# Kernel tuning notes

Measured on AMD Instinct MI355X. Metric: run time of the kernel, lower is better.

The kernel has to match this reference:

```python
import jax, jax.numpy as jnp
import numpy as np
from math import sqrt

B, MAXM, DIM, NH, QD, H, W = 8, 4, 128, 8, 16, 16, 16


def _pos_enc(h, w, max_m):
    # SE(2) positional phases: exp(i*m*theta_ij) for relative position j-i on the grid.
    ys, xs = jnp.meshgrid(jnp.arange(h, dtype=jnp.float32), jnp.arange(w, dtype=jnp.float32), indexing='ij')
    coords = jnp.stack([ys.ravel(), xs.ravel()], axis=-1)  # (N, 2)
    d = coords[None, :, :] - coords[:, None, :]            # (N, N, 2) = p_j - p_i
    theta = jnp.arctan2(d[..., 0], d[..., 1])              # (N, N)
    m = jnp.arange(max_m, dtype=jnp.float32)[:, None, None]
    return jnp.exp(1j * m * theta)                         # (max_m, N, N) complex64


def setup_inputs() -> dict:
    key = jax.random.key(0)
    ks = jax.random.split(key, 8)
    mk = lambda k, s: jax.random.normal(k, s, dtype=jnp.float32)
    return {
        'x_re': mk(ks[0], (B, MAXM, DIM, H, W)),
        'x_im': mk(ks[1], (B, MAXM, DIM, H, W)),
        'emb_re': mk(ks[2], (3, 1, MAXM, NH, QD, DIM)),
        'emb_im': mk(ks[3], (3, 1, MAXM, NH, QD, DIM)),
        'enc_re': mk(ks[4], (2, MAXM, NH, 1, QD, 1)),
        'enc_im': mk(ks[5], (2, MAXM, NH, 1, QD, 1)),
        'out_re': mk(ks[6], (MAXM, DIM, NH * QD)),
        'out_im': mk(ks[7], (MAXM, DIM, NH * QD)),
    }


def reference(x_re, x_im, emb_re, emb_im, enc_re, enc_im, out_re, out_im):
    x = (x_re + 1j * x_im)                         # (B, M, D, H, W) complex64
    b, m_, d_, h, w = x.shape
    n = h * w
    x = x.reshape(b, m_, d_, n)                    # (B, M, D, N)
    emb = (emb_re + 1j * emb_im)[:, 0]             # (3, M, NH, QD, D)
    enc = enc_re + 1j * enc_im                     # (2, M, NH, 1, QD, 1)
    w_out = out_re + 1j * out_im                   # (M, D, NH*QD)

    # E = embeddings @ x  -> (3, B, M, NH, QD, N)
    E = jnp.einsum('tmhqD,bmDn->tbmhqn', emb, x)
    E0, K, V = E[0], E[1], E[2]
    Q = jnp.conj(jnp.swapaxes(E0, -2, -1))         # (B, M, NH, N, QD)

    A = jnp.einsum('bmhiq,bmhqj->bmhij', Q, K)     # (B, M, NH, N, N)

    pe = _pos_enc(h, w, m_)                        # (M, N, N)
    enc0 = enc[0, :, :, 0, :, 0]                   # (M, NH, QD)
    enc1 = enc[1, :, :, 0, :, 0]                   # (M, NH, QD)
    # (Q.unsqueeze(-2) @ pos[0]).squeeze(-2) with pos[0][m,h,i,q,j] = enc0[m,h,q]*pe[m,i,j]
    QE = jnp.einsum('bmhiq,mhq->bmhi', Q, enc0)
    A = A + QE[..., None] * pe[None, :, None, :, :]

    A = jnp.sum(A, axis=1)                         # (B, NH, N, N)
    Aw = jax.nn.softmax(jnp.abs(A) / sqrt(QD), axis=-1).astype(jnp.complex64)
    # dropout is identity (eval / p effectively off for the reference)

    res = jnp.einsum('bmhqj,bhij->bmhqi', V, Aw)   # V @ A^T -> (B, M, NH, QD, N)
    # (pos[1] @ A.unsqueeze(-1)).squeeze(-1).T with pos[1][m,h,i,q,j] = enc1[m,h,q]*pe[m,i,j]
    PA = jnp.einsum('mij,bhij->bmhi', pe, Aw)
    res = res + enc1[None, :, :, :, None] * PA[:, :, :, None, :]

    res = res.reshape(b, m_, NH * QD, n)
    out = jnp.einsum('mDk,bmkn->bmDn', w_out, res).reshape(b, m_, d_, h, w)
    return jnp.stack([out.real, out.imag])         # (2, B, M, D, H, W) float32
```

## Files before the change

### kernel.cpp

```cpp
#include <hip/hip_runtime.h>
#include <math.h>

#define BB   8
#define MM   4
#define DD   128
#define NHH  8
#define QDD  16
#define NN   256
#define KO   128

typedef __attribute__((ext_vector_type(8))) short bf16x8;
typedef __attribute__((ext_vector_type(4))) float f32x4;

__device__ inline unsigned short f2bf(float f) {
    union { float f; unsigned u; } v; v.f = f;
    unsigned r = v.u + 0x7FFF + ((v.u >> 16) & 1);
    return (unsigned short)(r >> 16);
}
__device__ inline float bf2f(unsigned short h) {
    union { unsigned u; float f; } v; v.u = ((unsigned)h) << 16;
    return v.f;
}
__device__ inline void bfsplit(float x, unsigned short& hi, unsigned short& lo) {
    hi = f2bf(x);
    lo = f2bf(x - bf2f(hi));
}
__device__ inline bf16x8 derive_im(bf16x8 v) {
    union { bf16x8 v; unsigned u[4]; } in, out;
    in.v = v;
#pragma unroll
    for (int w = 0; w < 4; ++w)
        out.u[w] = ((in.u[w] >> 16) ^ 0x8000u) | (in.u[w] << 16);
    return out.v;
}
__device__ inline bf16x8 derive_im2(bf16x8 v) {
    union { bf16x8 v; unsigned u[4]; } in, out;
    in.v = v;
#pragma unroll
    for (int w = 0; w < 4; ++w)
        out.u[w] = (in.u[w] >> 16) | ((in.u[w] ^ 0x8000u) << 16);
    return out.v;
}

__global__ void pe_kernel(float2* __restrict__ peIJ) {
    int bid = blockIdx.x;
    int m = bid >> 8;
    int i = bid & 255;
    int j = threadIdx.x;
    float dy = (float)((j >> 4) - (i >> 4));
    float dx = (float)((j & 15) - (i & 15));
    float r2 = dx * dx + dy * dy;
    float c1 = 1.f, s1 = 0.f;
    if (r2 > 0.f) {
        float rinv = rsqrtf(r2);
        c1 = dx * rinv; s1 = dy * rinv;
    }
    float c = 1.f, s = 0.f;
    for (int k = 0; k < m; ++k) {
        float nc = c * c1 - s * s1;
        s = c * s1 + s * c1;
        c = nc;
    }
    peIJ[(m * NN + i) * NN + j] = make_float2(c, s);
}

__global__ void convAB_kernel(const float* __restrict__ er, const float* __restrict__ ei,
                              const float* __restrict__ xr, const float* __restrict__ xi,
                              const float* __restrict__ wor, const float* __restrict__ woi,
                              unsigned int* __restrict__ AbfHi, unsigned int* __restrict__ AbfLo,
                              unsigned int* __restrict__ BreHi, unsigned int* __restrict__ BreLo,
                              unsigned int* __restrict__ WFrag) {
    if (blockIdx.x < 96) {
        int tmh = blockIdx.x;
        int base = tmh * QDD * DD;
#pragma unroll
        for (int it = 0; it < 8; ++it) {
            int idx = threadIdx.x + it * 256;
            float ar = er[base + idx];
            float ai = ei[base + idx];
            unsigned short arh, arl, aih, ail;
            bfsplit(ar, arh, arl);
            bfsplit(ai, aih, ail);
            AbfHi[base + idx] = (unsigned int)arh | ((unsigned int)aih << 16);
            AbfLo[base + idx] = (unsigned int)arl | ((unsigned int)ail << 16);
        }
        return;
    }
    if (blockIdx.x >= 352) {
        int c = blockIdx.x - 352;
        int m = c >> 4;
        int dt = (c >> 1) & 7;
        int kshalf = c & 1;
        int tid = threadIdx.x;
        int wav = tid >> 6, lane = tid & 63;
        int ks = kshalf * 4 + wav;
        int D = dt * 16 + (lane & 15);
        unsigned int uu[8];
#pragma unroll
        for (int r = 0; r < 8; ++r) {
            int K2 = ks * 32 + ((lane >> 4) * 8) + r;
            int k = K2 >> 1;
            float v = (K2 & 1) ? woi[(m * DD + D) * KO + k] : wor[(m * DD + D) * KO + k];
            unsigned short hh, ll;
            bfsplit(v, hh, ll);
            uu[r] = (unsigned int)hh | ((unsigned int)ll << 16);
        }
        unsigned int* wp = WFrag + (((size_t)(m * 8 + dt) * 8 + ks) * 64 + lane) * 8;
        *(uint4*)wp = make_uint4(uu[0], uu[1], uu[2], uu[3]);
        *(uint4*)(wp + 4) = make_uint4(uu[4], uu[5], uu[6], uu[7]);
        return;
    }
    int bid = blockIdx.x - 96;
    int bm = bid >> 3;
    int Dg = bid & 7;
    int D0 = Dg * 16;
    int tid = threadIdx.x;

    __shared__ float sxr[16][257];
    __shared__ float sxi[16][257];

    const float* xrp = xr + (size_t)bm * DD * NN;
    const float* xip = xi + (size_t)bm * DD * NN;
#pragma unroll
    for (int it = 0; it < 16; ++it) {
        int i2 = tid + it * 256;
        int r = i2 >> 8, c = i2 & 255;
        sxr[r][c] = xrp[(size_t)(D0 + r) * NN + c];
        sxi[r][c] = xip[(size_t)(D0 + r) * NN + c];
    }
    __syncthreads();

    int n = tid;
    unsigned int reh[16], rel_[16];
#pragma unroll
    for (int d = 0; d < 16; ++d) {
        float br = sxr[d][n];
        float bi = sxi[d][n];
        unsigned short brh, brl, bih, bil;
        bfsplit(br, brh, brl);
        bfsplit(bi, bih, bil);
        reh[d]  = (unsigned int)brh | ((unsigned int)(bih ^ 0x8000) << 16);
        rel_[d] = (unsigned int)brl | ((unsigned int)(bil ^ 0x8000) << 16);
    }
    size_t ob = (size_t)bm * 32768 + (size_t)n * 128 + D0;
#pragma unroll
    for (int w = 0; w < 4; ++w) {
        ((uint4*)(BreHi + ob))[w] = make_uint4(reh[4*w], reh[4*w+1], reh[4*w+2], reh[4*w+3]);
        ((uint4*)(BreLo + ob))[w] = make_uint4(rel_[4*w], rel_[4*w+1], rel_[4*w+2], rel_[4*w+3]);
    }
}

__global__ __launch_bounds__(256, 2)
void e_mfma_kernel(const unsigned short* __restrict__ AbfHi,
                   const unsigned short* __restrict__ AbfLo,
                   const unsigned short* __restrict__ BreHi,
                   const unsigned short* __restrict__ BreLo,
                   const float* __restrict__ encr, const float* __restrict__ enci,
                   float2* __restrict__ E,
                   float2* __restrict__ QE,
                   unsigned int* __restrict__ EaHi, unsigned int* __restrict__ EaLo,
                   unsigned int* __restrict__ KbHi, unsigned int* __restrict__ KbLo) {
    int bid = blockIdx.x;
    int xcd = bid & 7;
    int idx = bid >> 3;
    int pair = xcd * 4 + (idx & 3);
    int h = (idx >> 2) & 7;
    int nhalf = idx >> 5;
    int b = pair >> 2, m = pair & 3;
    int tid = threadIdx.x;
    int wav = tid >> 6, lane = tid & 63;
    int lo = lane & 15, hi = lane >> 4;

    const unsigned short* AH[3];
    const unsigned short* AL[3];
#pragma unroll
    for (int t = 0; t < 3; ++t) {
        size_t aoff = ((size_t)((t * MM + m) * NHH + h)) * QDD * 256;
        AH[t] = AbfHi + aoff;
        AL[t] = AbfLo + aoff;
    }
    size_t boff = (size_t)pair * 256 * 256;
    const unsigned short* BrH = BreHi + boff;
    const unsigned short* BrL = BreLo + boff;

    f32x4 accRe[3][2], accIm[3][2];
#pragma unroll
    for (int t = 0; t < 3; ++t)
#pragma unroll
        for (int nt = 0; nt < 2; ++nt) {
            accRe[t][nt] = (f32x4)(0.f);
            accIm[t][nt] = (f32x4)(0.f);
        }

#pragma unroll
    for (int ks = 0; ks < 8; ++ks) {
        int k0 = ks * 32;
        int arow = lo * 256 + k0 + hi * 8;
        bf16x8 aH[3], aL[3];
#pragma unroll
        for (int t = 0; t < 3; ++t) {
            aH[t] = *(const bf16x8*)(AH[t] + arow);
            aL[t] = *(const bf16x8*)(AL[t] + arow);
        }
#pragma unroll
        for (int nt = 0; nt < 2; ++nt) {
            int n0 = nhalf * 128 + (wav * 2 + nt) * 16;
            size_t brow = (size_t)(n0 + lo) * 256 + k0 + hi * 8;
            bf16x8 brh = *(const bf16x8*)(BrH + brow);
            bf16x8 brl = *(const bf16x8*)(BrL + brow);
            bf16x8 bih = derive_im(brh);
            bf16x8 bil = derive_im(brl);
#pragma unroll
            for (int t = 0; t < 3; ++t) {
                accRe[t][nt] = __builtin_amdgcn_mfma_f32_16x16x32_bf16(aH[t], brh, accRe[t][nt], 0, 0, 0);
                accRe[t][nt] = __builtin_amdgcn_mfma_f32_16x16x32_bf16(aH[t], brl, accRe[t][nt], 0, 0, 0);
                accRe[t][nt] = __builtin_amdgcn_mfma_f32_16x16x32_bf16(aL[t], brh, accRe[t][nt], 0, 0, 0);
                accIm[t][nt] = __builtin_amdgcn_mfma_f32_16x16x32_bf16(aH[t], bih, accIm[t][nt], 0, 0, 0);
                accIm[t][nt] = __builtin_amdgcn_mfma_f32_16x16x32_bf16(aH[t], bil, accIm[t][nt], 0, 0, 0);
                accIm[t][nt] = __builtin_amdgcn_mfma_f32_16x16x32_bf16(aL[t], bih, accIm[t][nt], 0, 0, 0);
            }
        }
    }

    int bh = b * NHH + h;

    {
        float cr[4], ci[4];
#pragma unroll
        for (int reg = 0; reg < 4; ++reg) {
            int q = hi * 4 + reg;
            int eb = (m * NHH + h) * QDD + q;
            cr[reg] = encr[eb];
            ci[reg] = enci[eb];
        }
#pragma unroll
        for (int nt = 0; nt < 2; ++nt) {
            int n0 = nhalf * 128 + (wav * 2 + nt) * 16;
            float sr = 0.f, si = 0.f;
#pragma unroll
            for (int reg = 0; reg < 4; ++reg) {
                float erv = accRe[0][nt][reg];
                float eiv = accIm[0][nt][reg];
                sr = fmaf(erv, cr[reg], fmaf( eiv, ci[reg], sr));
                si = fmaf(erv, ci[reg], fmaf(-eiv, cr[reg], si));
            }
            sr += __shfl_xor(sr, 16); si += __shfl_xor(si, 16);
            sr += __shfl_xor(sr, 32); si += __shfl_xor(si, 32);
            if (hi == 0)
                QE[(size_t)((b * MM + m) * NHH + h) * NN + n0 + lo] = make_float2(sr, si);
        }
    }

#pragma unroll
    for (int t = 0; t < 3; ++t) {
        size_t ebase = (size_t)((((t * BB + b) * MM + m) * NHH + h) * QDD) * NN;
#pragma unroll
        for (int nt = 0; nt < 2; ++nt) {
            int n0 = nhalf * 128 + (wav * 2 + nt) * 16;
            if (t == 2) {
#pragma unroll
                for (int reg = 0; reg < 4; ++reg) {
                    int q = hi * 4 + reg;
                    E[ebase + (size_t)q * NN + n0 + lo] =
                        make_float2(accRe[t][nt][reg], accIm[t][nt][reg]);
                }
            }
            if (t < 2) {
                unsigned int hiU[4], loU[4];
#pragma unroll
                for (int reg = 0; reg < 4; ++reg) {
                    unsigned short rh, rl, ih, il;
                    bfsplit(accRe[t][nt][reg], rh, rl);
                    bfsplit(accIm[t][nt][reg], ih, il);
                    hiU[reg] = (unsigned int)rh | ((unsigned int)ih << 16);
                    loU[reg] = (unsigned int)rl | ((unsigned int)il << 16);
                }
                int r = n0 >> 4;
                size_t fo = (size_t)bh * 16384 + (size_t)((r * 4 + m) * 64 + lane) * 4;
                unsigned int* tH = (t == 0) ? EaHi : KbHi;
                unsigned int* tL = (t == 0) ? EaLo : KbLo;
                *(uint4*)(tH + fo) = make_uint4(hiU[0], hiU[1], hiU[2], hiU[3]);
                *(uint4*)(tL + fo) = make_uint4(loU[0], loU[1], loU[2], loU[3]);
            }
        }
    }
}

__global__ __launch_bounds__(256)
void score_kernel(const unsigned short* __restrict__ EaHi,
                  const unsigned short* __restrict__ EaLo,
                  const unsigned short* __restrict__ KbHi,
                  const unsigned short* __restrict__ KbLo,
                  const float2* __restrict__ QE,
                  const float2* __restrict__ peIJ,
                  unsigned int* __restrict__ AwFrag,
                  float2* __restrict__ PA) {
    int bid = blockIdx.x;
    int xcd = bid & 7;
    int idx = bid >> 3;
    int bh = xcd * 8 + (idx & 7);
    int it = idx >> 3;
    int b = bh >> 3, h = bh & 7;
    int tid = threadIdx.x;
    int wav = tid >> 6, lane = tid & 63;
    int lo = lane & 15, hi = lane >> 4;

    const unsigned short* EaH = EaHi + (size_t)bh * 32768;
    const unsigned short* EaL = EaLo + (size_t)bh * 32768;
    const unsigned short* KbH = KbHi + (size_t)bh * 32768;
    const unsigned short* KbL = KbLo + (size_t)bh * 32768;

    __shared__ float st[16][257];
    __shared__ float sredA[16][4];
    __shared__ float sredB[16][4];
    __shared__ float sPA[16][4][2][4];

    f32x4 accRe[4], accIm[4];
#pragma unroll
    for (int nt = 0; nt < 4; ++nt) { accRe[nt] = (f32x4)(0.f); accIm[nt] = (f32x4)(0.f); }

#pragma unroll
    for (int ks = 0; ks < 4; ++ks) {
        size_t arow = (size_t)((it * 4 + ks) * 64 + lane) * 8;
        bf16x8 aH = *(const bf16x8*)(EaH + arow);
        bf16x8 aL = *(const bf16x8*)(EaL + arow);
#pragma unroll
        for (int nt = 0; nt < 4; ++nt) {
            int jt = wav * 4 + nt;
            size_t brow = (size_t)((jt * 4 + ks) * 64 + lane) * 8;
            bf16x8 brh = *(const bf16x8*)(KbH + brow);
            bf16x8 brl = *(const bf16x8*)(KbL + brow);
            bf16x8 bih = derive_im2(brh);
            bf16x8 bil = derive_im2(brl);
            accRe[nt] = __builtin_amdgcn_mfma_f32_16x16x32_bf16(aH, brh, accRe[nt], 0, 0, 0);
            accRe[nt] = __builtin_amdgcn_mfma_f32_16x16x32_bf16(aH, brl, accRe[nt], 0, 0, 0);
            accRe[nt] = __builtin_amdgcn_mfma_f32_16x16x32_bf16(aL, brh, accRe[nt], 0, 0, 0);
            accIm[nt] = __builtin_amdgcn_mfma_f32_16x16x32_bf16(aH, bih, accIm[nt], 0, 0, 0);
            accIm[nt] = __builtin_amdgcn_mfma_f32_16x16x32_bf16(aH, bil, accIm[nt], 0, 0, 0);
            accIm[nt] = __builtin_amdgcn_mfma_f32_16x16x32_bf16(aL, bih, accIm[nt], 0, 0, 0);
        }
    }

    float vmag[4][4];
#pragma unroll
    for (int reg = 0; reg < 4; ++reg) {
        int i = it * 16 + hi * 4 + reg;
        float2 qe4[MM];
#pragma unroll
        for (int m = 0; m < MM; ++m)
            qe4[m] = QE[(size_t)((b * MM + m) * NHH + h) * NN + i];
#pragma unroll
        for (int nt = 0; nt < 4; ++nt) {
            int j = (wav * 4 + nt) * 16 + lo;
            float ar = accRe[nt][reg];
            float ai = accIm[nt][reg];
#pragma unroll
            for (int m = 0; m < MM; ++m) {
                float2 p = peIJ[(size_t)(m * NN + i) * NN + j];
                ar = fmaf(qe4[m].x, p.x, fmaf(-qe4[m].y, p.y, ar));
                ai = fmaf(qe4[m].x, p.y, fmaf( qe4[m].y, p.x, ai));
            }
            vmag[nt][reg] = sqrtf(fmaf(ar, ar, ai * ai)) * 0.25f;
        }
    }

    float mxr[4];
#pragma unroll
    for (int reg = 0; reg < 4; ++reg) {
        mxr[reg] = fmaxf(fmaxf(vmag[0][reg], vmag[1][reg]),
                         fmaxf(vmag[2][reg], vmag[3][reg]));
#pragma unroll
        for (int off = 1; off < 16; off <<= 1)
            mxr[reg] = fmaxf(mxr[reg], __shfl_xor(mxr[reg], off));
    }
    if (lo == 0) {
#pragma unroll
        for (int reg = 0; reg < 4; ++reg) sredA[hi * 4 + reg][wav] = mxr[reg];
    }
    __syncthreads();
    float mx[4];
#pragma unroll
    for (int reg = 0; reg < 4; ++reg) {
        int r = hi * 4 + reg;
        mx[reg] = fmaxf(fmaxf(sredA[r][0], sredA[r][1]),
                        fmaxf(sredA[r][2], sredA[r][3]));
    }

    float smr[4];
#pragma unroll
    for (int reg = 0; reg < 4; ++reg) smr[reg] = 0.f;
#pragma unroll
    for (int nt = 0; nt < 4; ++nt)
#pragma unroll
        for (int reg = 0; reg < 4; ++reg) {
            vmag[nt][reg] = __expf(vmag[nt][reg] - mx[reg]);
            smr[reg] += vmag[nt][reg];
        }
#pragma unroll
    for (int reg = 0; reg < 4; ++reg) {
#pragma unroll
        for (int off = 1; off < 16; off <<= 1)
            smr[reg] += __shfl_xor(smr[reg], off);
    }
    if (lo == 0) {
#pragma unroll
        for (int reg = 0; reg < 4; ++reg) sredB[hi * 4 + reg][wav] = smr[reg];
    }
    __syncthreads();
    float inv[4];
#pragma unroll
    for (int reg = 0; reg < 4; ++reg) {
        int r = hi * 4 + reg;
        inv[reg] = 1.f / (sredB[r][0] + sredB[r][1] + sredB[r][2] + sredB[r][3]);
    }

    float par[MM][4], pai[MM][4];
#pragma unroll
    for (int m = 0; m < MM; ++m)
#pragma unroll
        for (int reg = 0; reg < 4; ++reg) { par[m][reg] = 0.f; pai[m][reg] = 0.f; }
#pragma unroll
    for (int reg = 0; reg < 4; ++reg) {
        int i = it * 16 + hi * 4 + reg;
#pragma unroll
        for (int nt = 0; nt < 4; ++nt) {
            int j = (wav * 4 + nt) * 16 + lo;
            float aw = vmag[nt][reg] * inv[reg];
            st[hi * 4 + reg][j] = aw;
#pragma unroll
            for (int m = 0; m < MM; ++m) {
                float2 p = peIJ[(size_t)(m * NN + i) * NN + j];
                par[m][reg] = fmaf(p.x, aw, par[m][reg]);
                pai[m][reg] = fmaf(p.y, aw, pai[m][reg]);
            }
        }
    }
#pragma unroll
    for (int m = 0; m < MM; ++m)
#pragma unroll
        for (int reg = 0; reg < 4; ++reg) {
#pragma unroll
            for (int off = 1; off < 16; off <<= 1) {
                par[m][reg] += __shfl_xor(par[m][reg], off);
                pai[m][reg] += __shfl_xor(pai[m][reg], off);
            }
        }
    if (lo == 0) {
#pragma unroll
        for (int m = 0; m < MM; ++m)
#pragma unroll
            for (int reg = 0; reg < 4; ++reg) {
                sPA[hi * 4 + reg][m][0][wav] = par[m][reg];
                sPA[hi * 4 + reg][m][1][wav] = pai[m][reg];
            }
    }
    __syncthreads();

    if (tid < 16) {
        int r = tid;
#pragma unroll
        for (int m = 0; m < MM; ++m) {
            float pr  = sPA[r][m][0][0] + sPA[r][m][0][1] + sPA[r][m][0][2] + sPA[r][m][0][3];
            float pim = sPA[r][m][1][0] + sPA[r][m][1][1] + sPA[r][m][1][2] + sPA[r][m][1][3];
            PA[(size_t)((b * MM + m) * NHH + h) * NN + it * 16 + r] = make_float2(pr, pim);
        }
    }

#pragma unroll
    for (int ksl = 0; ksl < 2; ++ksl) {
        int ks = wav * 2 + ksl;
        unsigned int uu[8];
#pragma unroll
        for (int r = 0; r < 8; ++r) {
            float aw = st[lo][ks * 32 + hi * 8 + r];
            unsigned short h2, l2;
            bfsplit(aw, h2, l2);
            uu[r] = (unsigned int)h2 | ((unsigned int)l2 << 16);
        }
        unsigned int* ap = AwFrag + ((((size_t)bh * 16 + it) * 8 + ks) * 64 + lane) * 8;
        *(uint4*)ap = make_uint4(uu[0], uu[1], uu[2], uu[3]);
        *(uint4*)(ap + 4) = make_uint4(uu[4], uu[5], uu[6], uu[7]);
    }
}

__global__ __launch_bounds__(256, 2)
void res_mfma_kernel(const float2* __restrict__ E,
                     const unsigned int* __restrict__ AwFrag,
                     const float2* __restrict__ PA,
                     const float* __restrict__ encr, const float* __restrict__ enci,
                     unsigned int* __restrict__ ResFrag) {
    int bid = blockIdx.x;
    int xcd = bid & 7;
    int idx = bid >> 3;
    int bh = xcd * 8 + (idx & 7);
    int ih = idx >> 3;
    int b = bh >> 3, h = bh & 7;
    int tid = threadIdx.x;
    int m = tid >> 6;
    int lane = tid & 63;
    int lo = lane & 15, hi = lane >> 4;

    const float2* V = E + ((size_t)(((2 * BB + b) * MM + m) * NHH + h) * QDD) * NN;

    f32x4 accRe[2], accIm[2];
#pragma unroll
    for (int t2 = 0; t2 < 2; ++t2) { accRe[t2] = (f32x4)(0.f); accIm[t2] = (f32x4)(0.f); }

#pragma unroll
    for (int ks = 0; ks < 8; ++ks) {
        const float2* vp = V + (size_t)lo * NN + ks * 32 + hi * 8;
        union { bf16x8 v; unsigned short s[8]; } vrh, vrl, vih, vil;
#pragma unroll
        for (int r = 0; r < 8; ++r) {
            float2 v = vp[r];
            unsigned short rh, rl, ih2, il2;
            bfsplit(v.x, rh, rl);
            bfsplit(v.y, ih2, il2);
            vrh.s[r] = rh; vrl.s[r] = rl; vih.s[r] = ih2; vil.s[r] = il2;
        }
#pragma unroll
        for (int t2 = 0; t2 < 2; ++t2) {
            int it = ih * 2 + t2;
            const unsigned int* ap = AwFrag + ((((size_t)bh * 16 + it) * 8 + ks) * 64 + lane) * 8;
            uint4 u0 = *(const uint4*)ap;
            uint4 u1 = *(const uint4*)(ap + 4);
            unsigned int uu[8] = {u0.x, u0.y, u0.z, u0.w, u1.x, u1.y, u1.z, u1.w};
            union { bf16x8 v; unsigned short s[8]; } awh, awl;
#pragma unroll
            for (int r = 0; r < 8; ++r) {
                awh.s[r] = (unsigned short)(uu[r] & 0xffffu);
                awl.s[r] = (unsigned short)(uu[r] >> 16);
            }
            accRe[t2] = __builtin_amdgcn_mfma_f32_16x16x32_bf16(vrh.v, awh.v, accRe[t2], 0, 0, 0);
            accRe[t2] = __builtin_amdgcn_mfma_f32_16x16x32_bf16(vrh.v, awl.v, accRe[t2], 0, 0, 0);
            accRe[t2] = __builtin_amdgcn_mfma_f32_16x16x32_bf16(vrl.v, awh.v, accRe[t2], 0, 0, 0);
            accIm[t2] = __builtin_amdgcn_mfma_f32_16x16x32_bf16(vih.v, awh.v, accIm[t2], 0, 0, 0);
            accIm[t2] = __builtin_amdgcn_mfma_f32_16x16x32_bf16(vih.v, awl.v, accIm[t2], 0, 0, 0);
            accIm[t2] = __builtin_amdgcn_mfma_f32_16x16x32_bf16(vil.v, awh.v, accIm[t2], 0, 0, 0);
        }
    }

    float e1r[4], e1i[4];
#pragma unroll
    for (int reg = 0; reg < 4; ++reg) {
        int q = hi * 4 + reg;
        int eb = ((MM + m) * NHH + h) * QDD + q;
        e1r[reg] = encr[eb];
        e1i[reg] = enci[eb];
    }
    int bm = b * MM + m;
#pragma unroll
    for (int t2 = 0; t2 < 2; ++t2) {
        int nt = ih * 2 + t2;
        int i = nt * 16 + lo;
        float2 pa = PA[(size_t)((b * MM + m) * NHH + h) * NN + i];
        unsigned int uu[8];
#pragma unroll
        for (int reg = 0; reg < 4; ++reg) {
            float rr = accRe[t2][reg] + e1r[reg] * pa.x - e1i[reg] * pa.y;
            float ri = accIm[t2][reg] + e1r[reg] * pa.y + e1i[reg] * pa.x;
            unsigned short hh, ll;
            bfsplit(rr, hh, ll);
            uu[2 * reg] = (unsigned int)hh | ((unsigned int)ll << 16);
            bfsplit(-ri, hh, ll);
            uu[2 * reg + 1] = (unsigned int)hh | ((unsigned int)ll << 16);
        }
        unsigned int* rp = ResFrag + ((((size_t)bm * 16 + nt) * 8 + h) * 64 + lane) * 8;
        *(uint4*)rp = make_uint4(uu[0], uu[1], uu[2], uu[3]);
        *(uint4*)(rp + 4) = make_uint4(uu[4], uu[5], uu[6], uu[7]);
    }
}

__global__ __launch_bounds__(256, 2)
void out_mfma_kernel(const unsigned int* __restrict__ ResFrag,
                     const unsigned int* __restrict__ WFrag,
                     float* __restrict__ out) {
    int bid = blockIdx.x;
    int xcd = bid & 7;
    int idx = bid >> 3;
    int bm = xcd * 4 + (idx & 3);
    int rest = idx >> 2;
    int dt = rest >> 1;
    int nh = rest & 1;
    int m = bm & 3;
    int tid = threadIdx.x;
    int wav = tid >> 6, lane = tid & 63;
    int lo = lane & 15, hi = lane >> 4;

    f32x4 accRe[2], accIm[2];
#pragma unroll
    for (int t = 0; t < 2; ++t) { accRe[t] = (f32x4)(0.f); accIm[t] = (f32x4)(0.f); }

#pragma unroll
    for (int ks = 0; ks < 8; ++ks) {
        const unsigned int* wp = WFrag + (((size_t)(m * 8 + dt) * 8 + ks) * 64 + lane) * 8;
        uint4 w0 = *(const uint4*)wp;
        uint4 w1 = *(const uint4*)(wp + 4);
        unsigned int wu[8] = {w0.x, w0.y, w0.z, w0.w, w1.x, w1.y, w1.z, w1.w};
        union { bf16x8 v; unsigned short s[8]; } aH, aL;
#pragma unroll
        for (int r = 0; r < 8; ++r) {
            aH.s[r] = (unsigned short)(wu[r] & 0xffffu);
            aL.s[r] = (unsigned short)(wu[r] >> 16);
        }
#pragma unroll
        for (int nt2 = 0; nt2 < 2; ++nt2) {
            int nt = nh * 8 + wav * 2 + nt2;
            const unsigned int* rp = ResFrag + ((((size_t)bm * 16 + nt) * 8 + ks) * 64 + lane) * 8;
            uint4 r0 = *(const uint4*)rp;
            uint4 r1 = *(const uint4*)(rp + 4);
            unsigned int ru[8] = {r0.x, r0.y, r0.z, r0.w, r1.x, r1.y, r1.z, r1.w};
            union { bf16x8 v; unsigned short s[8]; } brH, brL, biH, biL;
#pragma unroll
            for (int t = 0; t < 4; ++t) {
                unsigned int ue = ru[2 * t], uo = ru[2 * t + 1];
                brH.s[2 * t]     = (unsigned short)(ue & 0xffffu);
                brL.s[2 * t]     = (unsigned short)(ue >> 16);
                brH.s[2 * t + 1] = (unsigned short)(uo & 0xffffu);
                brL.s[2 * t + 1] = (unsigned short)(uo >> 16);
                biH.s[2 * t]     = (unsigned short)((uo & 0xffffu) ^ 0x8000u);
                biL.s[2 * t]     = (unsigned short)((uo >> 16) ^ 0x8000u);
                biH.s[2 * t + 1] = (unsigned short)(ue & 0xffffu);
                biL.s[2 * t + 1] = (unsigned short)(ue >> 16);
            }
            accRe[nt2] = __builtin_amdgcn_mfma_f32_16x16x32_bf16(aH.v, brH.v, accRe[nt2], 0, 0, 0);
            accRe[nt2] = __builtin_amdgcn_mfma_f32_16x16x32_bf16(aH.v, brL.v, accRe[nt2], 0, 0, 0);
            accRe[nt2] = __builtin_amdgcn_mfma_f32_16x16x32_bf16(aL.v, brH.v, accRe[nt2], 0, 0, 0);
            accIm[nt2] = __builtin_amdgcn_mfma_f32_16x16x32_bf16(aH.v, biH.v, accIm[nt2], 0, 0, 0);
            accIm[nt2] = __builtin_amdgcn_mfma_f32_16x16x32_bf16(aH.v, biL.v, accIm[nt2], 0, 0, 0);
            accIm[nt2] = __builtin_amdgcn_mfma_f32_16x16x32_bf16(aL.v, biH.v, accIm[nt2], 0, 0, 0);
        }
    }

#pragma unroll
    for (int nt2 = 0; nt2 < 2; ++nt2) {
        int n = (nh * 8 + wav * 2 + nt2) * 16 + lo;
#pragma unroll
        for (int reg = 0; reg < 4; ++reg) {
            int D = dt * 16 + hi * 4 + reg;
            size_t ob = (size_t)(bm * DD + D) * NN + n;
            out[ob] = accRe[nt2][reg];
            out[(size_t)BB * MM * DD * NN + ob] = accIm[nt2][reg];
        }
    }
}

extern "C" void kernel_launch(void* const* d_in, const int* in_sizes, int n_in,
                              void* d_out, int out_size, void* d_ws, size_t ws_size,
                              hipStream_t stream) {
    (void)in_sizes; (void)n_in; (void)out_size; (void)ws_size;

    const float* x_re   = (const float*)d_in[0];
    const float* x_im   = (const float*)d_in[1];
    const float* emb_re = (const float*)d_in[2];
    const float* emb_im = (const float*)d_in[3];
    const float* enc_re = (const float*)d_in[4];
    const float* enc_im = (const float*)d_in[5];
    const float* out_re = (const float*)d_in[6];
    const float* out_im = (const float*)d_in[7];
    float* out = (float*)d_out;

    float* ws = (float*)d_ws;
    size_t off = 0;
    float2* peIJ = (float2*)(ws + off); off += (size_t)MM * NN * NN * 2;
    float*  peT  = (float*)(ws + off);  off += (size_t)MM * NN * NN * 2;
    float2* E    = (float2*)(ws + off); off += (size_t)3 * BB * MM * NHH * QDD * NN * 2;
    float2* QE   = (float2*)(ws + off); off += (size_t)BB * MM * NHH * NN * 2;
    float2* A    = (float2*)(ws + off); off += (size_t)BB * NHH * NN * NN * 2;
    float*  FRAG = (float*)(ws + off);  off += (size_t)BB * NHH * NN * NN;

    unsigned int* AbfHi = (unsigned int*)A;
    unsigned int* AbfLo = AbfHi + (size_t)96 * QDD * DD;
    unsigned int* BreHi = AbfLo + (size_t)96 * QDD * DD;
    unsigned int* BreLo = BreHi + (size_t)32 * 256 * 128;

    unsigned int* EaHi = (unsigned int*)FRAG;
    unsigned int* EaLo = EaHi + (size_t)64 * 16384;
    unsigned int* KbHi = EaLo + (size_t)64 * 16384;
    unsigned int* KbLo = KbHi + (size_t)64 * 16384;

    unsigned int* ResFrag = (unsigned int*)A;
    unsigned int* AwFrag  = (unsigned int*)((float*)A + (size_t)4194304);
    float2* PA    = (float2*)peT;
    unsigned int* WFrag = (unsigned int*)(peT + 262144);

    pe_kernel<<<MM * NN, 256, 0, stream>>>(peIJ);
    convAB_kernel<<<96 + 256 + 64, 256, 0, stream>>>(emb_re, emb_im, x_re, x_im,
                                                     out_re, out_im,
                                                     AbfHi, AbfLo, BreHi, BreLo, WFrag);
    e_mfma_kernel<<<512, 256, 0, stream>>>(
        (const unsigned short*)AbfHi, (const unsigned short*)AbfLo,
        (const unsigned short*)BreHi, (const unsigned short*)BreLo,
        enc_re, enc_im, E, QE,
        EaHi, EaLo, KbHi, KbLo);
    score_kernel<<<1024, 256, 0, stream>>>(
        (const unsigned short*)EaHi, (const unsigned short*)EaLo,
        (const unsigned short*)KbHi, (const unsigned short*)KbLo,
        QE, peIJ, AwFrag, PA);
    res_mfma_kernel<<<512, 256, 0, stream>>>(E, AwFrag, PA, enc_re, enc_im, ResFrag);
    out_mfma_kernel<<<512, 256, 0, stream>>>(ResFrag, WFrag, out);
}
```

Baseline: 98.61 us.

## Compute positional phases inline and pre-pack V into bf16 MFMA fragments

Removes the separate pe_kernel and its 2 MB phase table. The score kernel now computes exp(i*m*theta) on the fly from grid coordinates, using rsqrt and repeated complex multiplication instead of global loads. The E kernel also stages V through shared memory and writes it as pre-split hi/lo bf16 fragments, so the res kernel loads packed fragments rather than converting float2 V itself. This trades global memory traffic and one launch for extra ALU work in the score kernel and an added LDS pass plus barrier in the E kernel.

```diff
diff --git a/kernel.cpp b/kernel.cpp
--- a/kernel.cpp
+++ b/kernel.cpp
@@ -41,27 +41,15 @@
         out.u[w] = (in.u[w] >> 16) | ((in.u[w] ^ 0x8000u) << 16);
     return out.v;
 }
-
-__global__ void pe_kernel(float2* __restrict__ peIJ) {
-    int bid = blockIdx.x;
-    int m = bid >> 8;
-    int i = bid & 255;
-    int j = threadIdx.x;
+__device__ inline void pe_base(int i, int j, float& c1, float& s1) {
     float dy = (float)((j >> 4) - (i >> 4));
     float dx = (float)((j & 15) - (i & 15));
     float r2 = dx * dx + dy * dy;
-    float c1 = 1.f, s1 = 0.f;
+    c1 = 1.f; s1 = 0.f;
     if (r2 > 0.f) {
         float rinv = rsqrtf(r2);
         c1 = dx * rinv; s1 = dy * rinv;
     }
-    float c = 1.f, s = 0.f;
-    for (int k = 0; k < m; ++k) {
-        float nc = c * c1 - s * s1;
-        s = c * s1 + s * c1;
-        c = nc;
-    }
-    peIJ[(m * NN + i) * NN + j] = make_float2(c, s);
 }
 
 __global__ void convAB_kernel(const float* __restrict__ er, const float* __restrict__ ei,
@@ -156,10 +144,10 @@
                    const unsigned short* __restrict__ BreHi,
                    const unsigned short* __restrict__ BreLo,
                    const float* __restrict__ encr, const float* __restrict__ enci,
-                   float2* __restrict__ E,
                    float2* __restrict__ QE,
                    unsigned int* __restrict__ EaHi, unsigned int* __restrict__ EaLo,
-                   unsigned int* __restrict__ KbHi, unsigned int* __restrict__ KbLo) {
+                   unsigned int* __restrict__ KbHi, unsigned int* __restrict__ KbLo,
+                   unsigned int* __restrict__ VFragRe, unsigned int* __restrict__ VFragIm) {
     int bid = blockIdx.x;
     int xcd = bid & 7;
     int idx = bid >> 3;
@@ -171,6 +159,8 @@
     int wav = tid >> 6, lane = tid & 63;
     int lo = lane & 15, hi = lane >> 4;
 
+    __shared__ float2 sv[16][130];
+
     const unsigned short* AH[3];
     const unsigned short* AL[3];
 #pragma unroll
@@ -224,6 +214,14 @@
 
     int bh = b * NHH + h;
 
+#pragma unroll
+    for (int nt = 0; nt < 2; ++nt) {
+        int nl = (wav * 2 + nt) * 16;
+#pragma unroll
+        for (int reg = 0; reg < 4; ++reg)
+            sv[hi * 4 + reg][nl + lo] = make_float2(accRe[2][nt][reg], accIm[2][nt][reg]);
+    }
+
     {
         float cr[4], ci[4];
 #pragma unroll
@@ -252,37 +250,47 @@
     }
 
 #pragma unroll
-    for (int t = 0; t < 3; ++t) {
-        size_t ebase = (size_t)((((t * BB + b) * MM + m) * NHH + h) * QDD) * NN;
+    for (int t = 0; t < 2; ++t) {
 #pragma unroll
         for (int nt = 0; nt < 2; ++nt) {
             int n0 = nhalf * 128 + (wav * 2 + nt) * 16;
-            if (t == 2) {
-#pragma unroll
-                for (int reg = 0; reg < 4; ++reg) {
-                    int q = hi * 4 + reg;
-                    E[ebase + (size_t)q * NN + n0 + lo] =
-                        make_float2(accRe[t][nt][reg], accIm[t][nt][reg]);
-                }
-            }
-            if (t < 2) {
-                unsigned int hiU[4], loU[4];
-#pragma unroll
-                for (int reg = 0; reg < 4; ++reg) {
-                    unsigned short rh, rl, ih, il;
-                    bfsplit(accRe[t][nt][reg], rh, rl);
-                    bfsplit(accIm[t][nt][reg], ih, il);
-                    hiU[reg] = (unsigned int)rh | ((unsigned int)ih << 16);
-                    loU[reg] = (unsigned int)rl | ((unsigned int)il << 16);
-                }
-                int r = n0 >> 4;
-                size_t fo = (size_t)bh * 16384 + (size_t)((r * 4 + m) * 64 + lane) * 4;
-                unsigned int* tH = (t == 0) ? EaHi : KbHi;
-                unsigned int* tL = (t == 0) ? EaLo : KbLo;
-                *(uint4*)(tH + fo) = make_uint4(hiU[0], hiU[1], hiU[2], hiU[3]);
-                *(uint4*)(tL + fo) = make_uint4(loU[0], loU[1], loU[2], loU[3]);
-            }
-        }
+            unsigned int hiU[4], loU[4];
+#pragma unroll
+            for (int reg = 0; reg < 4; ++reg) {
+                unsigned short rh, rl, ih, il;
+                bfsplit(accRe[t][nt][reg], rh, rl);
+                bfsplit(accIm[t][nt][reg], ih, il);
+                hiU[reg] = (unsigned int)rh | ((unsigned int)ih << 16);
+                loU[reg] = (unsigned int)rl | ((unsigned int)il << 16);
+            }
+            int r = n0 >> 4;
+            size_t fo = (size_t)bh * 16384 + (size_t)((r * 4 + m) * 64 + lane) * 4;
+            unsigned int* tH = (t == 0) ? EaHi : KbHi;
+            unsigned int* tL = (t == 0) ? EaLo : KbLo;
+            *(uint4*)(tH + fo) = make_uint4(hiU[0], hiU[1], hiU[2], hiU[3]);
+            *(uint4*)(tL + fo) = make_uint4(loU[0], loU[1], loU[2], loU[3]);
+        }
+    }
+
+    __syncthreads();
+
+    {
+        int ks = nhalf * 4 + wav;
+        unsigned int uR[8], uI[8];
+#pragma unroll
+        for (int r = 0; r < 8; ++r) {
+            float2 v = sv[lo][wav * 32 + hi * 8 + r];
+            unsigned short rh, rl, ih2, il2;
+            bfsplit(v.x, rh, rl);
+            bfsplit(v.y, ih2, il2);
+            uR[r] = (unsigned int)rh | ((unsigned int)rl << 16);
+            uI[r] = (unsigned int)ih2 | ((unsigned int)il2 << 16);
+        }
+        size_t vo = ((((size_t)((b * MM + m) * NHH + h)) * 8 + ks) * 64 + lane) * 8;
+        *(uint4*)(VFragRe + vo)     = make_uint4(uR[0], uR[1], uR[2], uR[3]);
+        *(uint4*)(VFragRe + vo + 4) = make_uint4(uR[4], uR[5], uR[6], uR[7]);
+        *(uint4*)(VFragIm + vo)     = make_uint4(uI[0], uI[1], uI[2], uI[3]);
+        *(uint4*)(VFragIm + vo + 4) = make_uint4(uI[4], uI[5], uI[6], uI[7]);
     }
 }
 
@@ -292,7 +300,6 @@
                   const unsigned short* __restrict__ KbHi,
                   const unsigned short* __restrict__ KbLo,
                   const float2* __restrict__ QE,
-                  const float2* __restrict__ peIJ,
                   unsigned int* __restrict__ AwFrag,
                   float2* __restrict__ PA) {
     int bid = blockIdx.x;
@@ -352,13 +359,18 @@
 #pragma unroll
         for (int nt = 0; nt < 4; ++nt) {
             int j = (wav * 4 + nt) * 16 + lo;
+            float c1, s1;
+            pe_base(i, j, c1, s1);
             float ar = accRe[nt][reg];
             float ai = accIm[nt][reg];
+            float c = 1.f, s = 0.f;
 #pragma unroll
             for (int m = 0; m < MM; ++m) {
-                float2 p = peIJ[(size_t)(m * NN + i) * NN + j];
-                ar = fmaf(qe4[m].x, p.x, fmaf(-qe4[m].y, p.y, ar));
-                ai = fmaf(qe4[m].x, p.y, fmaf( qe4[m].y, p.x, ai));
+                ar = fmaf(qe4[m].x, c, fmaf(-qe4[m].y, s, ar));
+                ai = fmaf(qe4[m].x, s, fmaf( qe4[m].y, c, ai));
+                float nc = c * c1 - s * s1;
+                s = c * s1 + s * c1;
+                c = nc;
             }
             vmag[nt][reg] = sqrtf(fmaf(ar, ar, ai * ai)) * 0.25f;
         }
@@ -427,11 +439,16 @@
             int j = (wav * 4 + nt) * 16 + lo;
             float aw = vmag[nt][reg] * inv[reg];
             st[hi * 4 + reg][j] = aw;
+            float c1, s1;
+            pe_base(i, j, c1, s1);
+            float c = 1.f, s = 0.f;
 #pragma unroll
             for (int m = 0; m < MM; ++m) {
-                float2 p = peIJ[(size_t)(m * NN + i) * NN + j];
-                par[m][reg] = fmaf(p.x, aw, par[m][reg]);
-                pai[m][reg] = fmaf(p.y, aw, pai[m][reg]);
+                par[m][reg] = fmaf(c, aw, par[m][reg]);
+                pai[m][reg] = fmaf(s, aw, pai[m][reg]);
+                float nc = c * c1 - s * s1;
+                s = c * s1 + s * c1;
+                c = nc;
             }
         }
     }
@@ -484,7 +501,8 @@
 }
 
 __global__ __launch_bounds__(256, 2)
-void res_mfma_kernel(const float2* __restrict__ E,
+void res_mfma_kernel(const unsigned int* __restrict__ VFragRe,
+                     const unsigned int* __restrict__ VFragIm,
                      const unsigned int* __restrict__ AwFrag,
                      const float2* __restrict__ PA,
                      const float* __restrict__ encr, const float* __restrict__ enci,
@@ -500,23 +518,26 @@
     int lane = tid & 63;
     int lo = lane & 15, hi = lane >> 4;
 
-    const float2* V = E + ((size_t)(((2 * BB + b) * MM + m) * NHH + h) * QDD) * NN;
-
     f32x4 accRe[2], accIm[2];
 #pragma unroll
     for (int t2 = 0; t2 < 2; ++t2) { accRe[t2] = (f32x4)(0.f); accIm[t2] = (f32x4)(0.f); }
 
 #pragma unroll
     for (int ks = 0; ks < 8; ++ks) {
-        const float2* vp = V + (size_t)lo * NN + ks * 32 + hi * 8;
+        size_t vo = ((((size_t)((b * MM + m) * NHH + h)) * 8 + ks) * 64 + lane) * 8;
+        uint4 vr0 = *(const uint4*)(VFragRe + vo);
+        uint4 vr1 = *(const uint4*)(VFragRe + vo + 4);
+        uint4 vi0 = *(const uint4*)(VFragIm + vo);
+        uint4 vi1 = *(const uint4*)(VFragIm + vo + 4);
+        unsigned int uR[8] = {vr0.x, vr0.y, vr0.z, vr0.w, vr1.x, vr1.y, vr1.z, vr1.w};
+        unsigned int uI[8] = {vi0.x, vi0.y, vi0.z, vi0.w, vi1.x, vi1.y, vi1.z, vi1.w};
         union { bf16x8 v; unsigned short s[8]; } vrh, vrl, vih, vil;
 #pragma unroll
         for (int r = 0; r < 8; ++r) {
-            float2 v = vp[r];
-            unsigned short rh, rl, ih2, il2;
-            bfsplit(v.x, rh, rl);
-            bfsplit(v.y, ih2, il2);
-            vrh.s[r] = rh; vrl.s[r] = rl; vih.s[r] = ih2; vil.s[r] = il2;
+            vrh.s[r] = (unsigned short)(uR[r] & 0xffffu);
+            vrl.s[r] = (unsigned short)(uR[r] >> 16);
+            vih.s[r] = (unsigned short)(uI[r] & 0xffffu);
+            vil.s[r] = (unsigned short)(uI[r] >> 16);
         }
 #pragma unroll
         for (int t2 = 0; t2 < 2; ++t2) {
@@ -662,9 +683,9 @@
 
     float* ws = (float*)d_ws;
     size_t off = 0;
-    float2* peIJ = (float2*)(ws + off); off += (size_t)MM * NN * NN * 2;
+    off += (size_t)MM * NN * NN * 2;
     float*  peT  = (float*)(ws + off);  off += (size_t)MM * NN * NN * 2;
-    float2* E    = (float2*)(ws + off); off += (size_t)3 * BB * MM * NHH * QDD * NN * 2;
+    float*  Ereg = (float*)(ws + off);  off += (size_t)3 * BB * MM * NHH * QDD * NN * 2;
     float2* QE   = (float2*)(ws + off); off += (size_t)BB * MM * NHH * NN * 2;
     float2* A    = (float2*)(ws + off); off += (size_t)BB * NHH * NN * NN * 2;
     float*  FRAG = (float*)(ws + off);  off += (size_t)BB * NHH * NN * NN;
@@ -679,24 +700,27 @@
     unsigned int* KbHi = EaLo + (size_t)64 * 16384;
     unsigned int* KbLo = KbHi + (size_t)64 * 16384;
 
+    unsigned int* VFragRe = (unsigned int*)Ereg;
+    unsigned int* VFragIm = VFragRe + (size_t)1048576;
+
     unsigned int* ResFrag = (unsigned int*)A;
     unsigned int* AwFrag  = (unsigned int*)((float*)A + (size_t)4194304);
     float2* PA    = (float2*)peT;
     unsigned int* WFrag = (unsigned int*)(peT + 262144);
 
-    pe_kernel<<<MM * NN, 256, 0, stream>>>(peIJ);
     convAB_kernel<<<96 + 256 + 64, 256, 0, stream>>>(emb_re, emb_im, x_re, x_im,
                                                      out_re, out_im,
                                                      AbfHi, AbfLo, BreHi, BreLo, WFrag);
     e_mfma_kernel<<<512, 256, 0, stream>>>(
         (const unsigned short*)AbfHi, (const unsigned short*)AbfLo,
         (const unsigned short*)BreHi, (const unsigned short*)BreLo,
-        enc_re, enc_im, E, QE,
-        EaHi, EaLo, KbHi, KbLo);
+        enc_re, enc_im, QE,
+        EaHi, EaLo, KbHi, KbLo, VFragRe, VFragIm);
     score_kernel<<<1024, 256, 0, stream>>>(
         (const unsigned short*)EaHi, (const unsigned short*)EaLo,
         (const unsigned short*)KbHi, (const unsigned short*)KbLo,
-        QE, peIJ, AwFrag, PA);
-    res_mfma_kernel<<<512, 256, 0, stream>>>(E, AwFrag, PA, enc_re, enc_im, ResFrag);
+        QE, AwFrag, PA);
+    res_mfma_kernel<<<512, 256, 0, stream>>>(VFragRe, VFragIm, AwFrag, PA,
+                                             enc_re, enc_im, ResFrag);
     out_mfma_kernel<<<512, 256, 0, stream>>>(ResFrag, WFrag, out);
 }
```

Result: faster. 83.65 us (-15.2%).
